# Optimization experiments

Measured on AMD Instinct MI355X. Metric: run time of the kernel, lower is better.

The kernel has to match this reference:

```python
import jax, jax.numpy as jnp
import numpy as np

N, F = 4096, 255          # nodes, raw feature dim (one-hot adds +1 -> 256)
HID, D = 256, 256         # GCN hidden and out_dim
B, T, G = 8, 16384, 4     # n_breakings, n_tuples, n_groups
LN_EPS = 1e-5


def setup_inputs() -> dict:
    key = jax.random.key(0)
    ks = jax.random.split(key, 8)
    X = jax.random.normal(ks[0], (N, F), jnp.float32)
    adj_t = jax.random.uniform(ks[1], (N, N), jnp.float32)  # dense weighted adjacency
    W1 = jax.random.normal(ks[2], (F + 1, HID), jnp.float32) * 0.05
    b1 = jnp.zeros((HID,), jnp.float32)
    W2 = jax.random.normal(ks[3], (HID, D), jnp.float32) * 0.05
    b2 = jnp.zeros((D,), jnp.float32)
    ln_gamma = jnp.ones((D,), jnp.float32)
    ln_beta = jnp.zeros((D,), jnp.float32)
    tuples_coo = jax.random.randint(ks[4], (2, T), 0, N)
    group_idx = jax.random.randint(ks[5], (B,), 0, G)
    return dict(X=X, adj_t=adj_t, W1=W1, b1=b1, W2=W2, b2=b2,
                ln_gamma=ln_gamma, ln_beta=ln_beta,
                tuples_coo=tuples_coo, group_idx=group_idx,
                n_breakings=B, n_groups=G)


def reference(X, adj_t, W1, b1, W2, b2, ln_gamma, ln_beta,
              tuples_coo, group_idx, n_breakings, n_groups):
    n = X.shape[0]
    # --- symmetry breaking: top-k degree nodes (ties improbable for float degrees) ---
    deg = adj_t.sum(-1)                                   # [N]
    _, brk_idx = jax.lax.top_k(deg, n_breakings)          # [B]
    one_hot = jax.nn.one_hot(brk_idx, n, dtype=X.dtype)   # [B, N]
    # --- concat broadcast features with one-hot breaking channel ---
    Xin = jnp.concatenate(
        [jnp.broadcast_to(X[None], (n_breakings,) + X.shape), one_hot[..., None]],
        axis=-1)                                          # [B, N, F+1]
    # --- symmetry_breaking_model: 2-layer dense-adjacency GCN ---
    h = jax.nn.relu(jnp.einsum('nm,bmf->bnf', adj_t, Xin) @ W1 + b1)   # [B, N, HID]
    out = jnp.einsum('nm,bmf->bnf', adj_t, h) @ W2 + b2                # [B, N, D]
    # --- LayerNorm over feature dim ---
    mu = out.mean(-1, keepdims=True)
    var = out.var(-1, keepdims=True)
    holo = (out - mu) * jax.lax.rsqrt(var + LN_EPS) * ln_gamma + ln_beta  # [B, N, D]
    # --- gather tuple endpoints and reduce by product over arity ---
    gathered = holo[:, tuples_coo]                        # [B, arity, T, D]
    set_repr = gathered.prod(axis=1)                      # [B, T, D]
    # --- scatter-mean over breakings by group ---
    sums = jax.ops.segment_sum(set_repr, group_idx, num_segments=n_groups)  # [G, T, D]
    counts = jax.ops.segment_sum(jnp.ones((set_repr.shape[0],), set_repr.dtype),
                                 group_idx, num_segments=n_groups)          # [G]
    link = sums / jnp.maximum(counts, 1.0)[:, None, None]  # [G, T, D]
    # transpose(0,1).flatten(1,2): [T, G*D]
    return jnp.transpose(link, (1, 0, 2)).reshape(link.shape[1], -1)
```

## Files before the change

### kernel.cpp

```cpp
#include <hip/hip_runtime.h>
#include <hip/hip_bf16.h>

#define N_NODES 4096
#define FEAT    255
#define NB      8
#define NT      16384
#define NG      4

typedef __attribute__((ext_vector_type(8))) short          short8;
typedef __attribute__((ext_vector_type(8))) __bf16         bf16x8;
typedef __attribute__((ext_vector_type(4))) float          f32x4;
typedef __attribute__((ext_vector_type(4))) unsigned short ushort4v;

__device__ __forceinline__ unsigned short f2bf(float f) {
  unsigned int u = __builtin_bit_cast(unsigned int, f);
  u += 0x7fffu + ((u >> 16) & 1u);
  return (unsigned short)(u >> 16);
}

__device__ __forceinline__ f32x4 mfma16(short8 a, short8 b, f32x4 c) {
  return __builtin_amdgcn_mfma_f32_16x16x32_bf16(
      __builtin_bit_cast(bf16x8, a), __builtin_bit_cast(bf16x8, b), c, 0, 0, 0);
}

__device__ __forceinline__ void gload_lds16(const void* g, void* l) {
  __builtin_amdgcn_global_load_lds((__attribute__((address_space(1))) void*)(void*)g,
                                   (__attribute__((address_space(3))) void*)l, 16, 0, 0);
}

__global__ __launch_bounds__(256)
void deg_cvt(const float* __restrict__ adj, unsigned short* __restrict__ adjbf,
             float* __restrict__ deg)
{
  const int n = blockIdx.x;
  const int tid = threadIdx.x;
  const float* row = adj + (size_t)n * N_NODES;
  float s = 0.f;
#pragma unroll
  for (int it = 0; it < 4; ++it) {
    int idx = it * 1024 + tid * 4;
    float4 v = *(const float4*)(row + idx);
    s += (v.x + v.y) + (v.z + v.w);
    ushort4v o;
    o[0] = f2bf(v.x); o[1] = f2bf(v.y); o[2] = f2bf(v.z); o[3] = f2bf(v.w);
    *(ushort4v*)(adjbf + (size_t)n * N_NODES + idx) = o;
  }
#pragma unroll
  for (int off = 32; off > 0; off >>= 1) s += __shfl_xor(s, off);
  __shared__ float ws4[4];
  if ((tid & 63) == 0) ws4[tid >> 6] = s;
  __syncthreads();
  if (tid == 0) deg[n] = (ws4[0] + ws4[1]) + (ws4[2] + ws4[3]);
}

__global__ __launch_bounds__(256)
void topk_kernel(const float* __restrict__ deg, int* __restrict__ brk)
{
  __shared__ float v[N_NODES];
  __shared__ float wv[4];
  __shared__ int   wi[4];
  const int tid = threadIdx.x;
  for (int i = tid; i < N_NODES; i += 256) v[i] = deg[i];
  __syncthreads();
  for (int it = 0; it < NB; ++it) {
    float best = -1e30f; int bidx = 0x7fffffff;
#pragma unroll
    for (int k = 0; k < N_NODES / 256; ++k) {
      int i = k * 256 + tid;
      float x = v[i];
      if (x > best) { best = x; bidx = i; }
    }
#pragma unroll
    for (int off = 1; off < 64; off <<= 1) {
      float ov = __shfl_xor(best, off);
      int   oi = __shfl_xor(bidx, off);
      if (ov > best || (ov == best && oi < bidx)) { best = ov; bidx = oi; }
    }
    if ((tid & 63) == 0) { wv[tid >> 6] = best; wi[tid >> 6] = bidx; }
    __syncthreads();
    if (tid == 0) {
      float bb = wv[0]; int bbi = wi[0];
#pragma unroll
      for (int k = 1; k < 4; ++k)
        if (wv[k] > bb || (wv[k] == bb && wi[k] < bbi)) { bb = wv[k]; bbi = wi[k]; }
      brk[it] = bbi;
      v[bbi] = -1e30f;
    }
    __syncthreads();
  }
}

__global__ __launch_bounds__(256)
void extract_cols(const float* __restrict__ adj, const int* __restrict__ brk,
                  float* __restrict__ adjcol)
{
  const int n = blockIdx.x * 256 + threadIdx.x;
#pragma unroll
  for (int b = 0; b < NB; ++b)
    adjcol[b * N_NODES + n] = adj[(size_t)n * N_NODES + brk[b]];
}

__global__ __launch_bounds__(256)
void gemm0(const float* __restrict__ X, const float* __restrict__ W1,
           unsigned short* __restrict__ Yt)
{
  __shared__ float xr[FEAT];
  const int m = blockIdx.x;
  const int d = threadIdx.x;
  if (d < FEAT) xr[d] = X[(size_t)m * FEAT + d];
  __syncthreads();
  float s = 0.f;
#pragma unroll 5
  for (int f = 0; f < FEAT; ++f) s += xr[f] * W1[f * 256 + d];
  Yt[(size_t)d * N_NODES + m] = f2bf(s);
}

__global__ __launch_bounds__(256)
void w2t_kernel(const float* __restrict__ W2, unsigned short* __restrict__ W2t)
{
  const int k = blockIdx.x, d = threadIdx.x;
  W2t[(size_t)d * 256 + k] = f2bf(W2[(size_t)k * 256 + d]);
}

template<int BM, int BN, int BK, int FM, int FN>
__global__ __launch_bounds__(256)
void gemm_bt(const unsigned short* __restrict__ A, const unsigned short* __restrict__ Bt,
             float* __restrict__ C, int M, int Nn, int K)
{
  static_assert(BK == 64, "staging/swizzle math assumes BK=64 (128 B = 8 chunks/row)");
  __shared__ unsigned short As[BM * BK];
  __shared__ unsigned short Bs[BN * BK];
  const int tid  = threadIdx.x;
  const int lane = tid & 63;
  const int w    = tid >> 6;
  const int wr   = w >> 1, wc = w & 1;
  const int lhi  = lane >> 4, llo = lane & 15;
  const int brow = blockIdx.x * BM;
  const int bcol = blockIdx.y * BN;

  f32x4 acc[FM][FN];
  const f32x4 z = {0.f, 0.f, 0.f, 0.f};
#pragma unroll
  for (int m = 0; m < FM; ++m)
#pragma unroll
    for (int n = 0; n < FN; ++n) acc[m][n] = z;

  for (int k0 = 0; k0 < K; k0 += BK) {
    __syncthreads();
#pragma unroll
    for (int i = 0; i < (BM * BK * 2) / 4096; ++i) {
      int byte = i * 4096 + tid * 16;
      int row  = byte >> 7;
      int sc   = ((byte >> 4) & 7) ^ (row & 7);
      gload_lds16(A + (size_t)(brow + row) * K + k0 + sc * 8,
                  As + ((i * 4096 + w * 1024) >> 1));
    }
#pragma unroll
    for (int i = 0; i < (BN * BK * 2) / 4096; ++i) {
      int byte = i * 4096 + tid * 16;
      int row  = byte >> 7;
      int sc   = ((byte >> 4) & 7) ^ (row & 7);
      gload_lds16(Bt + (size_t)(bcol + row) * K + k0 + sc * 8,
                  Bs + ((i * 4096 + w * 1024) >> 1));
    }
    __syncthreads();
#pragma unroll
    for (int kk = 0; kk < BK; kk += 32) {
      short8 fa[FM], fb[FN];
#pragma unroll
      for (int m = 0; m < FM; ++m) {
        const int ar = wr * FM * 16 + m * 16 + llo;
        const int ac = ((kk >> 3) + lhi) ^ (ar & 7);
        fa[m] = *(const short8*)&As[ar * BK + ac * 8];
      }
#pragma unroll
      for (int n = 0; n < FN; ++n) {
        const int br = wc * FN * 16 + n * 16 + llo;
        const int bc = ((kk >> 3) + lhi) ^ (br & 7);
        fb[n] = *(const short8*)&Bs[br * BK + bc * 8];
      }
#pragma unroll
      for (int m = 0; m < FM; ++m)
#pragma unroll
        for (int n = 0; n < FN; ++n)
          acc[m][n] = mfma16(fa[m], fb[n], acc[m][n]);
    }
  }
#pragma unroll
  for (int m = 0; m < FM; ++m)
#pragma unroll
    for (int n = 0; n < FN; ++n) {
      const int r = brow + wr * FM * 16 + m * 16 + lhi * 4;
      const int c = bcol + wc * FN * 16 + n * 16 + llo;
      float* cp = C + (size_t)r * Nn + c;
#pragma unroll
      for (int i = 0; i < 4; ++i) cp[(size_t)i * Nn] = acc[m][n][i];
    }
}

__global__ __launch_bounds__(256)
void h_kernel(const float* __restrict__ base, const float* __restrict__ adjcol,
              const float* __restrict__ b1, const float* __restrict__ W1,
              unsigned short* __restrict__ Ht)
{
  __shared__ float bs[32][261];
  const int tid = threadIdx.x;
  const int m0  = blockIdx.x * 32;
  const int b   = blockIdx.y;
#pragma unroll
  for (int it = 0; it < 8; ++it) {
    int lin = it * 1024 + tid * 4;
    int mm = lin >> 8, d = lin & 255;
    float4 v = *(const float4*)(base + (size_t)(m0 + mm) * 256 + d);
    bs[mm][d] = v.x; bs[mm][d + 1] = v.y; bs[mm][d + 2] = v.z; bs[mm][d + 3] = v.w;
  }
  __syncthreads();
  const int ml = tid & 31, dg = tid >> 5;
  const float ac = adjcol[b * N_NODES + m0 + ml];
  const float* w1l = W1 + 255 * 256;
#pragma unroll 4
  for (int dd = 0; dd < 32; ++dd) {
    int d = dg * 32 + dd;
    float v = bs[ml][d] + b1[d] + ac * w1l[d];
    v = fmaxf(v, 0.f);
    Ht[(size_t)(b * 256 + d) * N_NODES + m0 + ml] = f2bf(v);
  }
}

__global__ __launch_bounds__(256)
void gemm3_ln(const float* __restrict__ Mcat, const unsigned short* __restrict__ W2t,
              const float* __restrict__ b2, const float* __restrict__ gamma,
              const float* __restrict__ beta, float* __restrict__ holo)
{
  const int tid  = threadIdx.x;
  const int w    = tid >> 6, lane = tid & 63;
  const int lhi  = lane >> 4, llo = lane & 15;
  const int n0   = blockIdx.x * 64;
  const int b    = blockIdx.y;
  const int row0 = n0 + w * 16;

  f32x4 acc[16];
  const f32x4 z = {0.f, 0.f, 0.f, 0.f};
#pragma unroll
  for (int j = 0; j < 16; ++j) acc[j] = z;

  const float* arow = Mcat + (size_t)(row0 + llo) * 2048 + b * 256;
#pragma unroll
  for (int k0 = 0; k0 < 256; k0 += 32) {
    const float4 a0 = *(const float4*)(arow + k0 + lhi * 8);
    const float4 a1 = *(const float4*)(arow + k0 + lhi * 8 + 4);
    float av[8] = {a0.x, a0.y, a0.z, a0.w, a1.x, a1.y, a1.z, a1.w};
    short8 fa;
#pragma unroll
    for (int i = 0; i < 8; ++i) fa[i] = (short)f2bf(av[i]);
#pragma unroll
    for (int j = 0; j < 16; ++j) {
      const short8 fb = *(const short8*)&W2t[(size_t)(j * 16 + llo) * 256 + k0 + lhi * 8];
      acc[j] = mfma16(fa, fb, acc[j]);
    }
  }
  float b2v[16];
#pragma unroll
  for (int j = 0; j < 16; ++j) b2v[j] = b2[j * 16 + llo];

  float mu[4], rs[4];
#pragma unroll
  for (int i = 0; i < 4; ++i) {
    float s = 0.f;
#pragma unroll
    for (int j = 0; j < 16; ++j) s += acc[j][i] + b2v[j];
    s += __shfl_xor(s, 1); s += __shfl_xor(s, 2);
    s += __shfl_xor(s, 4); s += __shfl_xor(s, 8);
    mu[i] = s * (1.f / 256.f);
  }
#pragma unroll
  for (int i = 0; i < 4; ++i) {
    float q = 0.f;
#pragma unroll
    for (int j = 0; j < 16; ++j) { float d = acc[j][i] + b2v[j] - mu[i]; q += d * d; }
    q += __shfl_xor(q, 1); q += __shfl_xor(q, 2);
    q += __shfl_xor(q, 4); q += __shfl_xor(q, 8);
    rs[i] = rsqrtf(q * (1.f / 256.f) + 1e-5f);
  }
  float* hb = holo + ((size_t)b * N_NODES + row0 + lhi * 4) * 256 + llo;
#pragma unroll
  for (int j = 0; j < 16; ++j) {
    const float gv = gamma[j * 16 + llo];
    const float bt = beta[j * 16 + llo];
#pragma unroll
    for (int i = 0; i < 4; ++i) {
      float x = acc[j][i] + b2v[j];
      hb[(size_t)i * 256 + j * 16] = (x - mu[i]) * rs[i] * gv + bt;
    }
  }
}

__global__ __launch_bounds__(256)
void gather_k(const float* __restrict__ holo, const int* __restrict__ tc,
              const int* __restrict__ gidx, float* __restrict__ out)
{
  const int t = blockIdx.x;
  const int d = threadIdx.x;
  const int i = tc[t];
  const int j = tc[NT + t];
  float a0 = 0.f, a1 = 0.f, a2 = 0.f, a3 = 0.f;
  float c0 = 0.f, c1 = 0.f, c2 = 0.f, c3 = 0.f;
#pragma unroll
  for (int b = 0; b < NB; ++b) {
    const int g = gidx[b];
    const float p = holo[((size_t)b * N_NODES + i) * 256 + d] *
                    holo[((size_t)b * N_NODES + j) * 256 + d];
    a0 += (g == 0) ? p : 0.f;  c0 += (g == 0) ? 1.f : 0.f;
    a1 += (g == 1) ? p : 0.f;  c1 += (g == 1) ? 1.f : 0.f;
    a2 += (g == 2) ? p : 0.f;  c2 += (g == 2) ? 1.f : 0.f;
    a3 += (g == 3) ? p : 0.f;  c3 += (g == 3) ? 1.f : 0.f;
  }
  float* ob = out + (size_t)t * 1024 + d;
  ob[0]   = a0 / fmaxf(c0, 1.f);
  ob[256] = a1 / fmaxf(c1, 1.f);
  ob[512] = a2 / fmaxf(c2, 1.f);
  ob[768] = a3 / fmaxf(c3, 1.f);
}

extern "C" void kernel_launch(void* const* d_in, const int* in_sizes, int n_in,
                              void* d_out, int out_size, void* d_ws, size_t ws_size,
                              hipStream_t stream)
{
  const float* X     = (const float*)d_in[0];
  const float* adj   = (const float*)d_in[1];
  const float* W1    = (const float*)d_in[2];
  const float* b1    = (const float*)d_in[3];
  const float* W2    = (const float*)d_in[4];
  const float* b2    = (const float*)d_in[5];
  const float* gamma = (const float*)d_in[6];
  const float* beta  = (const float*)d_in[7];
  const int*   tc    = (const int*)d_in[8];
  const int*   gidx  = (const int*)d_in[9];

  char* w = (char*)d_ws;
  size_t off = 0;
  unsigned short* adjbf = (unsigned short*)(w + off);
  float*          holo  = (float*)(w + off);  off += 33554432;
  unsigned short* Ht    = (unsigned short*)(w + off); off += 16777216;
  float*          Mcat  = (float*)(w + off);  off += 33554432;
  float*          base  = (float*)(w + off);  off += 4194304;
  unsigned short* Yt    = (unsigned short*)(w + off); off += 2097152;
  float*          deg   = (float*)(w + off);  off += 16384;
  int*            brk   = (int*)(w + off);    off += 256;
  float*          adjcol= (float*)(w + off);  off += 131072;
  unsigned short* W2t   = (unsigned short*)(w + off); off += 131072;
  float* out = (float*)d_out;

  deg_cvt     <<<N_NODES, 256, 0, stream>>>(adj, adjbf, deg);
  topk_kernel <<<1, 256, 0, stream>>>(deg, brk);
  extract_cols<<<N_NODES / 256, 256, 0, stream>>>(adj, brk, adjcol);
  gemm0       <<<N_NODES, 256, 0, stream>>>(X, W1, Yt);
  w2t_kernel  <<<256, 256, 0, stream>>>(W2, W2t);
  gemm_bt<64, 64, 64, 2, 2>  <<<dim3(N_NODES / 64, 256 / 64), 256, 0, stream>>>(
      adjbf, Yt, base, N_NODES, 256, N_NODES);
  h_kernel    <<<dim3(N_NODES / 32, NB), 256, 0, stream>>>(base, adjcol, b1, W1, Ht);
  gemm_bt<128, 128, 64, 4, 4><<<dim3(N_NODES / 128, 2048 / 128), 256, 0, stream>>>(
      adjbf, Ht, Mcat, N_NODES, 2048, N_NODES);
  gemm3_ln    <<<dim3(N_NODES / 64, NB), 256, 0, stream>>>(Mcat, W2t, b2, gamma, beta, holo);
  gather_k    <<<NT, 256, 0, stream>>>(holo, tc, gidx, out);
}
```

Measured before the change: 412.2 us.

## Split-K first adjacency GEMM, bf16 Mcat output, and register-block gemm0 rows

The first adjacency GEMM (N=256 output) now splits K four ways across grid z into partial buffers, with a new reduce4 kernel summing them. This raises the block count from 256 to 1024 to fill the GPU. The big GEMM now writes Mcat in bf16, which halves its store traffic and lets gemm3_ln load bf16 directly without converting. gemm0 computes 8 rows per block so each W1 load is reused across rows. The costs are an extra kernel launch plus partial-sum traffic. Rounding is unchanged, since Mcat was already rounded to bf16 before its MFMA.

Result: faster. 374.8 us (-9.1%).

```diff
diff --git a/kernel.cpp b/kernel.cpp
--- a/kernel.cpp
+++ b/kernel.cpp
@@ -100,19 +100,43 @@
     adjcol[b * N_NODES + n] = adj[(size_t)n * N_NODES + brk[b]];
 }
 
+#define G0R 8
 __global__ __launch_bounds__(256)
 void gemm0(const float* __restrict__ X, const float* __restrict__ W1,
            unsigned short* __restrict__ Yt)
 {
-  __shared__ float xr[FEAT];
-  const int m = blockIdx.x;
-  const int d = threadIdx.x;
-  if (d < FEAT) xr[d] = X[(size_t)m * FEAT + d];
+  __shared__ float xr[G0R][256];
+  const int tid = threadIdx.x;
+  const int m0  = blockIdx.x * G0R;
+  for (int i = tid; i < G0R * FEAT; i += 256) {
+    int r = i / FEAT, c = i - r * FEAT;
+    xr[r][c] = X[(size_t)(m0 + r) * FEAT + c];
+  }
   __syncthreads();
-  float s = 0.f;
-#pragma unroll 5
-  for (int f = 0; f < FEAT; ++f) s += xr[f] * W1[f * 256 + d];
-  Yt[(size_t)d * N_NODES + m] = f2bf(s);
+  const int d = tid;
+  float s[G0R] = {};
+  for (int fq = 0; fq < 252; fq += 4) {
+    float w0 = W1[(fq + 0) * 256 + d];
+    float w1 = W1[(fq + 1) * 256 + d];
+    float w2 = W1[(fq + 2) * 256 + d];
+    float w3 = W1[(fq + 3) * 256 + d];
+#pragma unroll
+    for (int r = 0; r < G0R; ++r) {
+      float4 x4 = *(const float4*)&xr[r][fq];
+      s[r] = fmaf(x4.x, w0, s[r]);
+      s[r] = fmaf(x4.y, w1, s[r]);
+      s[r] = fmaf(x4.z, w2, s[r]);
+      s[r] = fmaf(x4.w, w3, s[r]);
+    }
+  }
+  for (int f = 252; f < FEAT; ++f) {
+    float wv = W1[f * 256 + d];
+#pragma unroll
+    for (int r = 0; r < G0R; ++r) s[r] = fmaf(xr[r][f], wv, s[r]);
+  }
+#pragma unroll
+  for (int r = 0; r < G0R; ++r)
+    Yt[(size_t)d * N_NODES + m0 + r] = f2bf(s[r]);
 }
 
 __global__ __launch_bounds__(256)
@@ -122,10 +146,10 @@
   W2t[(size_t)d * 256 + k] = f2bf(W2[(size_t)k * 256 + d]);
 }
 
-template<int BM, int BN, int BK, int FM, int FN>
+template<int BM, int BN, int BK, int FM, int FN, bool OUTBF>
 __global__ __launch_bounds__(256)
 void gemm_bt(const unsigned short* __restrict__ A, const unsigned short* __restrict__ Bt,
-             float* __restrict__ C, int M, int Nn, int K)
+             void* __restrict__ Cv, int M, int Nn, int K)
 {
   static_assert(BK == 64, "staging/swizzle math assumes BK=64 (128 B = 8 chunks/row)");
   __shared__ unsigned short As[BM * BK];
@@ -137,6 +161,8 @@
   const int lhi  = lane >> 4, llo = lane & 15;
   const int brow = blockIdx.x * BM;
   const int bcol = blockIdx.y * BN;
+  const int Kper = K / gridDim.z;
+  const int kbeg = blockIdx.z * Kper;
 
   f32x4 acc[FM][FN];
   const f32x4 z = {0.f, 0.f, 0.f, 0.f};
@@ -145,7 +171,7 @@
 #pragma unroll
     for (int n = 0; n < FN; ++n) acc[m][n] = z;
 
-  for (int k0 = 0; k0 < K; k0 += BK) {
+  for (int k0 = kbeg; k0 < kbeg + Kper; k0 += BK) {
     __syncthreads();
 #pragma unroll
     for (int i = 0; i < (BM * BK * 2) / 4096; ++i) {
@@ -192,10 +218,34 @@
     for (int n = 0; n < FN; ++n) {
       const int r = brow + wr * FM * 16 + m * 16 + lhi * 4;
       const int c = bcol + wc * FN * 16 + n * 16 + llo;
-      float* cp = C + (size_t)r * Nn + c;
-#pragma unroll
-      for (int i = 0; i < 4; ++i) cp[(size_t)i * Nn] = acc[m][n][i];
-    }
+      if constexpr (OUTBF) {
+        unsigned short* cp = (unsigned short*)Cv + (size_t)blockIdx.z * M * Nn
+                             + (size_t)r * Nn + c;
+#pragma unroll
+        for (int i = 0; i < 4; ++i) cp[(size_t)i * Nn] = f2bf(acc[m][n][i]);
+      } else {
+        float* cp = (float*)Cv + (size_t)blockIdx.z * M * Nn + (size_t)r * Nn + c;
+#pragma unroll
+        for (int i = 0; i < 4; ++i) cp[(size_t)i * Nn] = acc[m][n][i];
+      }
+    }
+}
+
+__global__ __launch_bounds__(256)
+void reduce4(const float* __restrict__ bp, float* __restrict__ base)
+{
+  const size_t i = (size_t)blockIdx.x * 256 + threadIdx.x;
+  const float4* b0 = (const float4*)bp;
+  const float4* b1 = b0 + (size_t)N_NODES * 256 / 4;
+  const float4* b2 = b1 + (size_t)N_NODES * 256 / 4;
+  const float4* b3 = b2 + (size_t)N_NODES * 256 / 4;
+  float4 v0 = b0[i], v1 = b1[i], v2 = b2[i], v3 = b3[i];
+  float4 o;
+  o.x = ((v0.x + v1.x) + v2.x) + v3.x;
+  o.y = ((v0.y + v1.y) + v2.y) + v3.y;
+  o.z = ((v0.z + v1.z) + v2.z) + v3.z;
+  o.w = ((v0.w + v1.w) + v2.w) + v3.w;
+  ((float4*)base)[i] = o;
 }
 
 __global__ __launch_bounds__(256)
@@ -228,7 +278,7 @@
 }
 
 __global__ __launch_bounds__(256)
-void gemm3_ln(const float* __restrict__ Mcat, const unsigned short* __restrict__ W2t,
+void gemm3_ln(const unsigned short* __restrict__ Mcat, const unsigned short* __restrict__ W2t,
               const float* __restrict__ b2, const float* __restrict__ gamma,
               const float* __restrict__ beta, float* __restrict__ holo)
 {
@@ -244,15 +294,10 @@
 #pragma unroll
   for (int j = 0; j < 16; ++j) acc[j] = z;
 
-  const float* arow = Mcat + (size_t)(row0 + llo) * 2048 + b * 256;
+  const unsigned short* arow = Mcat + (size_t)(row0 + llo) * 2048 + b * 256;
 #pragma unroll
   for (int k0 = 0; k0 < 256; k0 += 32) {
-    const float4 a0 = *(const float4*)(arow + k0 + lhi * 8);
-    const float4 a1 = *(const float4*)(arow + k0 + lhi * 8 + 4);
-    float av[8] = {a0.x, a0.y, a0.z, a0.w, a1.x, a1.y, a1.z, a1.w};
-    short8 fa;
-#pragma unroll
-    for (int i = 0; i < 8; ++i) fa[i] = (short)f2bf(av[i]);
+    const short8 fa = *(const short8*)&arow[k0 + lhi * 8];
 #pragma unroll
     for (int j = 0; j < 16; ++j) {
       const short8 fb = *(const short8*)&W2t[(size_t)(j * 16 + llo) * 256 + k0 + lhi * 8];
@@ -342,7 +387,8 @@
   unsigned short* adjbf = (unsigned short*)(w + off);
   float*          holo  = (float*)(w + off);  off += 33554432;
   unsigned short* Ht    = (unsigned short*)(w + off); off += 16777216;
-  float*          Mcat  = (float*)(w + off);  off += 33554432;
+  unsigned short* Mcat  = (unsigned short*)(w + off); off += 16777216;
+  float*          basep = (float*)(w + off);  off += 16777216;
   float*          base  = (float*)(w + off);  off += 4194304;
   unsigned short* Yt    = (unsigned short*)(w + off); off += 2097152;
   float*          deg   = (float*)(w + off);  off += 16384;
@@ -354,12 +400,13 @@
   deg_cvt     <<<N_NODES, 256, 0, stream>>>(adj, adjbf, deg);
   topk_kernel <<<1, 256, 0, stream>>>(deg, brk);
   extract_cols<<<N_NODES / 256, 256, 0, stream>>>(adj, brk, adjcol);
-  gemm0       <<<N_NODES, 256, 0, stream>>>(X, W1, Yt);
+  gemm0       <<<N_NODES / G0R, 256, 0, stream>>>(X, W1, Yt);
   w2t_kernel  <<<256, 256, 0, stream>>>(W2, W2t);
-  gemm_bt<64, 64, 64, 2, 2>  <<<dim3(N_NODES / 64, 256 / 64), 256, 0, stream>>>(
-      adjbf, Yt, base, N_NODES, 256, N_NODES);
+  gemm_bt<64, 64, 64, 2, 2, false><<<dim3(N_NODES / 64, 256 / 64, 4), 256, 0, stream>>>(
+      adjbf, Yt, basep, N_NODES, 256, N_NODES);
+  reduce4     <<<N_NODES * 256 / 4 / 256, 256, 0, stream>>>(basep, base);
   h_kernel    <<<dim3(N_NODES / 32, NB), 256, 0, stream>>>(base, adjcol, b1, W1, Ht);
-  gemm_bt<128, 128, 64, 4, 4><<<dim3(N_NODES / 128, 2048 / 128), 256, 0, stream>>>(
+  gemm_bt<128, 128, 64, 4, 4, true><<<dim3(N_NODES / 128, 2048 / 128, 1), 256, 0, stream>>>(
       adjbf, Ht, Mcat, N_NODES, 2048, N_NODES);
   gemm3_ln    <<<dim3(N_NODES / 64, NB), 256, 0, stream>>>(Mcat, W2t, b2, gamma, beta, holo);
   gather_k    <<<NT, 256, 0, stream>>>(holo, tc, gidx, out);
```
